# Kernel optimization log

Measured on AMD Instinct MI355X. Metric: run time of the kernel, lower is better.

## Reference

```python
import jax, jax.numpy as jnp
import numpy as np

BITWIDTH = 4  # sqllm 4-bit packing: 8 codes per int32


def sqllm_dequant4(qweight, lut):
    # qweight: [num_int32s, N] int32 (stored packed); lut: [N, 16]
    qw = qweight.T  # [N, num_int32s]
    shifts = jnp.arange(8, dtype=jnp.int32) * 4  # [8]
    # extract 8 nibbles per int32 -> indices in [0, 16)
    idx = (qw[:, :, None] >> shifts[None, None, :]) & 15  # [N, num_int32s, 8]
    N = qw.shape[0]
    idx = idx.reshape(N, -1)  # [N, K] with K = num_int32s * 8
    return jnp.take_along_axis(lut, idx, axis=1)  # [N, K]


def setup_inputs() -> dict:
    key = jax.random.key(0)
    k1, k2, k3 = jax.random.split(key, 3)
    B, S, K, N = 4, 2048, 4096, 4096
    inp = {
        "input": jax.random.normal(k1, (B, S, K), dtype=jnp.float32),
        "qweight": jax.random.randint(k2, (K // 8, N), 0, 2147483647, dtype=jnp.int32),
        "lut": jax.random.normal(k3, (N, 16), dtype=jnp.float32),
    }
    return inp


def reference(input, qweight, lut):
    # sqllm_gemm: dequantize packed 4-bit weights via LUT gather, then input @ W.T
    weights = sqllm_dequant4(qweight, lut)  # [N, K]
    return jnp.einsum("bsk,nk->bsn", input, weights)  # [B, S, N]
```

## Files before the change

kernel.cpp:

```cpp
#include <hip/hip_runtime.h>
#include <hip/hip_bf16.h>


typedef __attribute__((ext_vector_type(4))) float  f32x4;
typedef __attribute__((ext_vector_type(4))) int    i32x4;
typedef __attribute__((ext_vector_type(8))) short  bf16x8;

__device__ __forceinline__ unsigned short f2bf(float f) {
    __hip_bfloat16 h = __float2bfloat16(f);
    return __builtin_bit_cast(unsigned short, h);
}

__device__ __forceinline__ void gload16(const unsigned short* g, unsigned short* l) {
    __builtin_amdgcn_global_load_lds(
        (const __attribute__((address_space(1))) unsigned int*)g,
        (__attribute__((address_space(3))) unsigned int*)l, 16, 0, 0);
}


__global__ void convA_kernel(const float* __restrict__ in, unsigned short* __restrict__ o, long n8) {
    long i = (long)blockIdx.x * blockDim.x + threadIdx.x;
    long stride = (long)gridDim.x * blockDim.x;
    const f32x4* in4 = reinterpret_cast<const f32x4*>(in);
    bf16x8* o8 = reinterpret_cast<bf16x8*>(o);
    for (; i < n8; i += stride) {
        f32x4 a = in4[2 * i];
        f32x4 b = in4[2 * i + 1];
        bf16x8 e;
#pragma unroll
        for (int x = 0; x < 4; ++x) {
            e[x]     = (short)f2bf(a[x]);
            e[4 + x] = (short)f2bf(b[x]);
        }
        o8[i] = e;
    }
}

__global__ void dequantW_kernel(const int* __restrict__ Q, const float* __restrict__ lut,
                                unsigned short* __restrict__ Wb, int N, long total) {
    long i = (long)blockIdx.x * blockDim.x + threadIdx.x;
    if (i >= total) return;
    unsigned int v = (unsigned int)Q[i];
    int n = (int)(i % N);
    const float* lp = lut + (long)n * 16;
    bf16x8 w;
#pragma unroll
    for (int p = 0; p < 8; ++p)
        w[p] = (short)f2bf(lp[(v >> (4 * p)) & 15]);
    reinterpret_cast<bf16x8*>(Wb)[i] = w;
}


#define LOADFRAGS(NA, NB, SLOT) do {                                              \
    const unsigned short* SA_ = sA + (SLOT) * 8192;                               \
    const unsigned short* SB_ = sB + (SLOT) * 8192;                               \
    _Pragma("unroll") for (int nf = 0; nf < 4; ++nf)                              \
        NB[nf] = *(const bf16x8*)(SB_ + boff + nf * 128);                         \
    _Pragma("unroll") for (int mf = 0; mf < 8; ++mf)                              \
        NA[mf] = *(const bf16x8*)(SA_ + aoff + mf * 512);                         \
} while (0)

#define MFMABLOCK(CA, CB)                                                         \
    _Pragma("unroll") for (int mf = 0; mf < 8; ++mf)                              \
        _Pragma("unroll") for (int nf = 0; nf < 4; ++nf)                          \
            acc[mf][nf] = __builtin_amdgcn_mfma_f32_16x16x32_bf16(                \
                CA[mf], CB[nf], acc[mf][nf], 0, 0, 0);

#define PHASE(U, CA, CB, NA, NB) do {                                             \
    int S = H + (U) + 3; if (S >= NH) S -= NH;                                    \
    stage(S, ((U) + 3) & 3);                                                      \
    LOADFRAGS(NA, NB, ((U) + 1) & 3);                                             \
    __builtin_amdgcn_s_setprio(1);                                                \
    MFMABLOCK(CA, CB)                                                             \
    __builtin_amdgcn_s_setprio(0);                                                \
    asm volatile("s_waitcnt vmcnt(4)" ::: "memory");                              \
    __builtin_amdgcn_s_barrier();                                                 \
} while (0)

__global__ __launch_bounds__(512, 2)
void gemm8p(const unsigned short* __restrict__ Abf, const unsigned short* __restrict__ Wb,
            float* __restrict__ out, int M, int N, int K) {
    __shared__ __align__(16) unsigned short sA[4 * 8192];
    __shared__ __align__(16) unsigned short sB[4 * 8192];

    const int tid  = threadIdx.x;
    const int lane = tid & 63;
    const int wid  = tid >> 6;
    const int wr   = wid >> 2;
    const int wc   = wid & 3;
    const int r15  = lane & 15;
    const int hi   = lane >> 4;

    int nwg = gridDim.x, orig = blockIdx.x;
    int wg = ((nwg & 7) == 0) ? (orig & 7) * (nwg >> 3) + (orig >> 3) : orig;
    const int NBN = N / 256;
    const int m0 = (wg / NBN) * 256, n0 = (wg % NBN) * 256;

    const int NH = K / 32;

    const int aoff = (wr * 128 + r15) * 32 + ((hi ^ ((r15 >> 1) & 3)) << 3);
    const int boff = hi * 2048 + (wc * 64 + r15) * 8;

    const int am  = tid >> 2, akc = tid & 3;
    const int akcs = (akc ^ ((am >> 1) & 3)) << 3;
    const unsigned short* baseA0 = Abf + (size_t)(m0 + am) * K + akcs;
    const unsigned short* baseA1 = Abf + (size_t)(m0 + am + 128) * K + akcs;
    const int bkc = tid >> 8, bn = tid & 255;
    const unsigned short* baseB0 = Wb + ((size_t)bkc * N + n0 + bn) * 8;
    const unsigned short* baseB1 = Wb + ((size_t)(bkc + 2) * N + n0 + bn) * 8;
    const size_t bstride = (size_t)32 * N;
    unsigned short* const dA = sA + wid * 512;
    unsigned short* const dB = sB + wid * 512;

    auto stage = [&](int S, int slot) {
        gload16(baseA0 + S * 32, dA + slot * 8192);
        gload16(baseB0 + S * bstride, dB + slot * 8192);
        gload16(baseA1 + S * 32, dA + slot * 8192 + 4096);
        gload16(baseB1 + S * bstride, dB + slot * 8192 + 4096);
    };

    f32x4 acc[8][4] = {};
    bf16x8 avA[8], bvA[4], avB[8], bvB[4];

    stage(0, 0);
    stage(1, 1);
    stage(2, 2);
    asm volatile("s_waitcnt vmcnt(4)" ::: "memory");
    __builtin_amdgcn_s_barrier();
    LOADFRAGS(avA, bvA, 0);

    for (int H = 0; H < NH; H += 4) {
        PHASE(0, avA, bvA, avB, bvB);
        PHASE(1, avB, bvB, avA, bvA);
        PHASE(2, avA, bvA, avB, bvB);
        PHASE(3, avB, bvB, avA, bvA);
    }

    asm volatile("s_waitcnt vmcnt(0)" ::: "memory");

#pragma unroll
    for (int mf = 0; mf < 8; ++mf) {
        const int mrow = m0 + wr * 128 + mf * 16 + hi * 4;
#pragma unroll
        for (int nf = 0; nf < 4; ++nf) {
            const int ncol = n0 + wc * 64 + nf * 16 + r15;
            float* po = out + (size_t)mrow * N + ncol;
#pragma unroll
            for (int r = 0; r < 4; ++r) po[(size_t)r * N] = acc[mf][nf][r];
        }
    }
}

#undef PHASE
#undef MFMABLOCK
#undef LOADFRAGS


#define FBM 128
#define FBN 128
#define FBK 64

__device__ __forceinline__ int fswz(int row, int kb) {
    return row * (FBK * 2) + (kb ^ ((row & 7) << 4));
}

__global__ __launch_bounds__(256, 2)
void sqllm_gemm_fused(const float* __restrict__ A, const int* __restrict__ Q,
                      const float* __restrict__ lut, float* __restrict__ out,
                      int M, int N, int K) {
    __shared__ __align__(16) char sA[FBM * FBK * 2];
    __shared__ __align__(16) char sB[FBN * FBK * 2];
    __shared__ float sLut[FBN * 17];

    const int tid  = threadIdx.x;
    const int lane = tid & 63;
    const int wid  = tid >> 6;
    const int wr   = wid >> 1;
    const int wc   = wid & 1;
    const int n0 = blockIdx.x * FBN;
    const int m0 = blockIdx.y * FBM;

    for (int i = tid; i < FBN * 16; i += 256) {
        int n = i >> 4, c = i & 15;
        sLut[n * 17 + c] = lut[(long)(n0 + n) * 16 + c];
    }
    __syncthreads();

    f32x4 acc[4][4] = {};
    const int nK = K / FBK;
    for (int kk = 0; kk < nK; ++kk) {
        {
            const int r = tid >> 1, h = tid & 1;
            const float* ap = A + (long)(m0 + r) * K + kk * FBK + h * 32;
            f32x4 v[8];
#pragma unroll
            for (int j = 0; j < 8; ++j) v[j] = reinterpret_cast<const f32x4*>(ap)[j];
            const int kr = tid >> 5, nq = (tid & 31) << 2;
            const int* qp = Q + (long)(kk * (FBK / 8) + kr) * N + n0 + nq;
            i32x4 q = *reinterpret_cast<const i32x4*>(qp);
#pragma unroll
            for (int j = 0; j < 4; ++j) {
                bf16x8 e;
#pragma unroll
                for (int x = 0; x < 4; ++x) {
                    e[x]     = (short)f2bf(v[2 * j][x]);
                    e[4 + x] = (short)f2bf(v[2 * j + 1][x]);
                }
                *reinterpret_cast<bf16x8*>(sA + fswz(r, h * 64 + j * 16)) = e;
            }
#pragma unroll
            for (int c = 0; c < 4; ++c) {
                const int n = nq + c;
                const float* lp = sLut + n * 17;
                unsigned int qq = (unsigned int)q[c];
                bf16x8 w;
#pragma unroll
                for (int p = 0; p < 8; ++p)
                    w[p] = (short)f2bf(lp[(qq >> (4 * p)) & 15]);
                *reinterpret_cast<bf16x8*>(sB + fswz(n, kr * 16)) = w;
            }
        }
        __syncthreads();
#pragma unroll
        for (int kh = 0; kh < 2; ++kh) {
            const int kb = kh * 64 + (lane >> 4) * 16;
            bf16x8 af[4], bfv[4];
#pragma unroll
            for (int i = 0; i < 4; ++i) {
                af[i]  = *reinterpret_cast<const bf16x8*>(sA + fswz(wr * 64 + i * 16 + (lane & 15), kb));
                bfv[i] = *reinterpret_cast<const bf16x8*>(sB + fswz(wc * 64 + i * 16 + (lane & 15), kb));
            }
#pragma unroll
            for (int i = 0; i < 4; ++i)
#pragma unroll
                for (int j = 0; j < 4; ++j)
                    acc[i][j] = __builtin_amdgcn_mfma_f32_16x16x32_bf16(af[i], bfv[j], acc[i][j], 0, 0, 0);
        }
        __syncthreads();
    }
    const int col = lane & 15;
    const int r4  = (lane >> 4) * 4;
#pragma unroll
    for (int i = 0; i < 4; ++i) {
        const int mrow = m0 + wr * 64 + i * 16 + r4;
#pragma unroll
        for (int j = 0; j < 4; ++j) {
            const int ncol = n0 + wc * 64 + j * 16 + col;
#pragma unroll
            for (int r = 0; r < 4; ++r)
                out[(long)(mrow + r) * N + ncol] = acc[i][j][r];
        }
    }
}

extern "C" void kernel_launch(void* const* d_in, const int* in_sizes, int n_in,
                              void* d_out, int out_size, void* d_ws, size_t ws_size,
                              hipStream_t stream) {
    const float* A   = (const float*)d_in[0];
    const int*   Q   = (const int*)d_in[1];
    const float* lut = (const float*)d_in[2];
    float* out = (float*)d_out;

    const long szA = in_sizes[0], szQ = in_sizes[1], szL = in_sizes[2];
    const int N = (int)(szL / 16);
    const int K = (int)(szQ * 8 / N);
    const int M = (int)(szA / K);

    const size_t needA = (size_t)M * K * 2;
    const size_t needW = (size_t)K * N * 2;

    const bool shape_ok = (M % 256 == 0) && (N % 256 == 0) && (K % 128 == 0);

    if (shape_ok && ws_size >= needA + needW) {
        unsigned short* Abf = (unsigned short*)d_ws;
        unsigned short* Wb  = (unsigned short*)((char*)d_ws + needA);
        const long n8 = (long)M * K / 8;
        convA_kernel<<<2048, 256, 0, stream>>>(A, Abf, n8);
        const long tq = (long)(K / 8) * N;
        dequantW_kernel<<<(int)((tq + 255) / 256), 256, 0, stream>>>(Q, lut, Wb, N, tq);
        dim3 grid((M / 256) * (N / 256));
        gemm8p<<<grid, 512, 0, stream>>>(Abf, Wb, out, M, N, K);
    } else {
        dim3 grid(N / FBN, M / FBM);
        sqllm_gemm_fused<<<grid, 256, 0, stream>>>(A, Q, lut, out, M, N, K);
    }
}
```

Measured before the change: 294.0 us.

## Restructure GEMM main loop into half-tile sub-phases with split staging

Replaces the double-buffered register fragment pipeline (full 8x4 MFMA block per K step with prefetch of next fragments) with sub-phases that each load four A fragments (and B on alternating halves), then barrier, wait on LDS and run 16 MFMAs. Global-to-LDS staging is split into two halves interleaved across sub-phases, and barriers bracket each compute cluster in a ping-pong style schedule. This aims to cut register pressure and interleave memory issue with MFMA more evenly. The cost is many more barriers per K step and the loss of LDS-read/MFMA overlap within a wave.

```diff
diff --git a/kernel.cpp b/kernel.cpp
--- a/kernel.cpp
+++ b/kernel.cpp
@@ -51,30 +51,47 @@
 }
 
 
-#define LOADFRAGS(NA, NB, SLOT) do {                                              \
-    const unsigned short* SA_ = sA + (SLOT) * 8192;                               \
-    const unsigned short* SB_ = sB + (SLOT) * 8192;                               \
-    _Pragma("unroll") for (int nf = 0; nf < 4; ++nf)                              \
-        NB[nf] = *(const bf16x8*)(SB_ + boff + nf * 128);                         \
-    _Pragma("unroll") for (int mf = 0; mf < 8; ++mf)                              \
-        NA[mf] = *(const bf16x8*)(SA_ + aoff + mf * 512);                         \
+#define MFMA4(MF, AF) \
+    acc[MF][0] = __builtin_amdgcn_mfma_f32_16x16x32_bf16(AF, bv0, acc[MF][0], 0, 0, 0); \
+    acc[MF][1] = __builtin_amdgcn_mfma_f32_16x16x32_bf16(AF, bv1, acc[MF][1], 0, 0, 0); \
+    acc[MF][2] = __builtin_amdgcn_mfma_f32_16x16x32_bf16(AF, bv2, acc[MF][2], 0, 0, 0); \
+    acc[MF][3] = __builtin_amdgcn_mfma_f32_16x16x32_bf16(AF, bv3, acc[MF][3], 0, 0, 0);
+
+#define SPH(SLOT, MB, LOADB, STG, WAITSTMT) do {                               \
+    const unsigned short* SA_ = sA + (SLOT) * 8192;                            \
+    if (LOADB) {                                                               \
+        const unsigned short* SB_ = sB + (SLOT) * 8192;                        \
+        bv0 = *(const bf16x8*)(SB_ + boff + 0 * 128);                          \
+        bv1 = *(const bf16x8*)(SB_ + boff + 1 * 128);                          \
+        bv2 = *(const bf16x8*)(SB_ + boff + 2 * 128);                          \
+        bv3 = *(const bf16x8*)(SB_ + boff + 3 * 128);                          \
+    }                                                                          \
+    bf16x8 a0_ = *(const bf16x8*)(SA_ + aoff + ((MB) + 0) * 512);              \
+    bf16x8 a1_ = *(const bf16x8*)(SA_ + aoff + ((MB) + 1) * 512);              \
+    bf16x8 a2_ = *(const bf16x8*)(SA_ + aoff + ((MB) + 2) * 512);              \
+    bf16x8 a3_ = *(const bf16x8*)(SA_ + aoff + ((MB) + 3) * 512);              \
+    STG;                                                                       \
+    WAITSTMT;                                                                  \
+    __builtin_amdgcn_s_barrier();                                              \
+    asm volatile("s_waitcnt lgkmcnt(0)" ::: "memory");                         \
+    __builtin_amdgcn_sched_barrier(0);                                         \
+    __builtin_amdgcn_s_setprio(1);                                             \
+    MFMA4((MB) + 0, a0_)                                                       \
+    MFMA4((MB) + 1, a1_)                                                       \
+    MFMA4((MB) + 2, a2_)                                                       \
+    MFMA4((MB) + 3, a3_)                                                       \
+    __builtin_amdgcn_s_setprio(0);                                             \
+    __builtin_amdgcn_s_barrier();                                              \
 } while (0)
 
-#define MFMABLOCK(CA, CB)                                                         \
-    _Pragma("unroll") for (int mf = 0; mf < 8; ++mf)                              \
-        _Pragma("unroll") for (int nf = 0; nf < 4; ++nf)                          \
-            acc[mf][nf] = __builtin_amdgcn_mfma_f32_16x16x32_bf16(                \
-                CA[mf], CB[nf], acc[mf][nf], 0, 0, 0);
-
-#define PHASE(U, CA, CB, NA, NB) do {                                             \
-    int S = H + (U) + 3; if (S >= NH) S -= NH;                                    \
-    stage(S, ((U) + 3) & 3);                                                      \
-    LOADFRAGS(NA, NB, ((U) + 1) & 3);                                             \
-    __builtin_amdgcn_s_setprio(1);                                                \
-    MFMABLOCK(CA, CB)                                                             \
-    __builtin_amdgcn_s_setprio(0);                                                \
-    asm volatile("s_waitcnt vmcnt(4)" ::: "memory");                              \
-    __builtin_amdgcn_s_barrier();                                                 \
+#define DPH(S0, S1, H3, H4) do {                                               \
+    int S3_ = (H3) >= NH ? (H3) - NH : (H3);                                   \
+    int S4_ = (H4) >= NH ? (H4) - NH : (H4);                                   \
+    SPH(S0, 0, 1, stageP1(S3_, ((S0) + 3) & 3), );                             \
+    SPH(S0, 4, 0, stageP2(S3_, ((S0) + 3) & 3), );                             \
+    SPH(S1, 0, 1, stageP1(S4_, (S0)), );                                       \
+    SPH(S1, 4, 0, stageP2(S4_, (S0)),                                          \
+        asm volatile("s_waitcnt vmcnt(4)" ::: "memory"));                      \
 } while (0)
 
 __global__ __launch_bounds__(512, 2)
@@ -91,9 +108,9 @@
     const int r15  = lane & 15;
     const int hi   = lane >> 4;
 
+    const int NBN = N / 256;
     int nwg = gridDim.x, orig = blockIdx.x;
     int wg = ((nwg & 7) == 0) ? (orig & 7) * (nwg >> 3) + (orig >> 3) : orig;
-    const int NBN = N / 256;
     const int m0 = (wg / NBN) * 256, n0 = (wg % NBN) * 256;
 
     const int NH = K / 32;
@@ -112,28 +129,27 @@
     unsigned short* const dA = sA + wid * 512;
     unsigned short* const dB = sB + wid * 512;
 
-    auto stage = [&](int S, int slot) {
+    auto stageP1 = [&](int S, int slot) {
         gload16(baseA0 + S * 32, dA + slot * 8192);
         gload16(baseB0 + S * bstride, dB + slot * 8192);
+    };
+    auto stageP2 = [&](int S, int slot) {
         gload16(baseA1 + S * 32, dA + slot * 8192 + 4096);
         gload16(baseB1 + S * bstride, dB + slot * 8192 + 4096);
     };
 
     f32x4 acc[8][4] = {};
-    bf16x8 avA[8], bvA[4], avB[8], bvB[4];
-
-    stage(0, 0);
-    stage(1, 1);
-    stage(2, 2);
+    bf16x8 bv0, bv1, bv2, bv3;
+
+    stageP1(0, 0); stageP2(0, 0);
+    stageP1(1, 1); stageP2(1, 1);
+    stageP1(2, 2); stageP2(2, 2);
     asm volatile("s_waitcnt vmcnt(4)" ::: "memory");
     __builtin_amdgcn_s_barrier();
-    LOADFRAGS(avA, bvA, 0);
-
-    for (int H = 0; H < NH; H += 4) {
-        PHASE(0, avA, bvA, avB, bvB);
-        PHASE(1, avB, bvB, avA, bvA);
-        PHASE(2, avA, bvA, avB, bvB);
-        PHASE(3, avB, bvB, avA, bvA);
+
+    for (int h = 0; h < NH; h += 4) {
+        DPH(0, 1, h + 3, h + 4);
+        DPH(2, 3, h + 5, h + 6);
     }
 
     asm volatile("s_waitcnt vmcnt(0)" ::: "memory");
@@ -151,9 +167,9 @@
     }
 }
 
-#undef PHASE
-#undef MFMABLOCK
-#undef LOADFRAGS
+#undef DPH
+#undef SPH
+#undef MFMA4
 
 
 #define FBM 128
```

New measurement: 303.7 us. 1.03x slower.
